# Kernel optimization log

Measured on AMD Instinct MI355X. Metric: run time of the kernel, lower is better.

Reference implementation:

```python
import jax, jax.numpy as jnp
import numpy as np

DIM = 192
HEADS = 6
WSIZE = (2, 8, 8)
SSIZE = (1, 4, 4)
HID = 768
EPS = 1e-5


def _rel_pos_index(ws):
    d, h, w = ws
    coords = np.stack(np.meshgrid(np.arange(d), np.arange(h), np.arange(w), indexing='ij'))
    cf = coords.reshape(3, -1)                       # (3, N)
    rel = (cf[:, :, None] - cf[:, None, :]).transpose(1, 2, 0)  # (N, N, 3)
    rel[:, :, 0] += d - 1
    rel[:, :, 1] += h - 1
    rel[:, :, 2] += w - 1
    rel[:, :, 0] *= (2 * h - 1) * (2 * w - 1)
    rel[:, :, 1] *= 2 * w - 1
    return rel.sum(-1)                               # (N, N) int


def _slices(w, s):
    if s == 0:
        return [slice(0, None)]
    return [slice(0, -w), slice(-w, -s), slice(-s, None)]


def _window_partition(x, ws):
    B, D, H, W, C = x.shape
    x = x.reshape(B, D // ws[0], ws[0], H // ws[1], ws[1], W // ws[2], ws[2], C)
    return x.transpose(0, 1, 3, 5, 2, 4, 6, 7).reshape(-1, ws[0] * ws[1] * ws[2], C)


def _window_reverse(win, ws, B, D, H, W):
    x = win.reshape(B, D // ws[0], H // ws[1], W // ws[2], ws[0], ws[1], ws[2], -1)
    return x.transpose(0, 1, 4, 2, 5, 3, 6, 7).reshape(B, D, H, W, -1)


def _compute_mask(D, H, W, ws, ss):
    img = np.zeros((1, D, H, W, 1), np.float32)
    cnt = 0
    for d in _slices(ws[0], ss[0]):
        for h in _slices(ws[1], ss[1]):
            for w in _slices(ws[2], ss[2]):
                img[:, d, h, w, :] = cnt
                cnt += 1
    x = img.reshape(1, D // ws[0], ws[0], H // ws[1], ws[1], W // ws[2], ws[2], 1)
    mw = x.transpose(0, 1, 3, 5, 2, 4, 6, 7).reshape(-1, ws[0] * ws[1] * ws[2])  # (nW, N)
    diff = mw[:, None, :] - mw[:, :, None]
    return np.where(diff != 0, np.float32(-100.0), np.float32(0.0))  # (nW, N, N)


def _ln(x, g, b):
    mu = x.mean(-1, keepdims=True)
    v = ((x - mu) ** 2).mean(-1, keepdims=True)
    return (x - mu) * jax.lax.rsqrt(v + EPS) * g + b


def setup_inputs() -> dict:
    key = jax.random.key(0)
    ks = jax.random.split(key, 8)
    C, H_, n_bias = DIM, HID, (2 * WSIZE[0] - 1) * (2 * WSIZE[1] - 1) * (2 * WSIZE[2] - 1)
    s = 0.02
    return {
        'x': jax.random.normal(ks[0], (2, 8, 64, 64, C), jnp.float32),
        'g1': jnp.ones((C,), jnp.float32), 'b1': jnp.zeros((C,), jnp.float32),
        'Wq': jax.random.normal(ks[1], (C, C), jnp.float32) * s,
        'Wkv': jax.random.normal(ks[2], (2 * C, C), jnp.float32) * s,
        'rpb': jax.random.normal(ks[3], (n_bias, HEADS), jnp.float32) * s,
        'Wp': jax.random.normal(ks[4], (C, C), jnp.float32) * s,
        'bp': jnp.zeros((C,), jnp.float32),
        'g2': jnp.ones((C,), jnp.float32), 'b2': jnp.zeros((C,), jnp.float32),
        'Wf1': jax.random.normal(ks[5], (H_, C), jnp.float32) * s,
        'bf1': jnp.zeros((H_,), jnp.float32),
        'Wf2': jax.random.normal(ks[6], (C, H_), jnp.float32) * s,
        'bf2': jnp.zeros((C,), jnp.float32),
    }


def reference(x, g1, b1, Wq, Wkv, rpb, Wp, bp, g2, b2, Wf1, bf1, Wf2, bf2):
    B, D, H, W, C = x.shape
    ws, ss = list(WSIZE), list(SSIZE)
    for i, sz in enumerate((D, H, W)):
        if sz <= ws[i]:
            ws[i], ss[i] = sz, 0
    shortcut = x
    x = _ln(x, g1, b1)
    # pad to window multiples
    pd, ph, pw = (-D) % ws[0], (-H) % ws[1], (-W) % ws[2]
    x = jnp.pad(x, ((0, 0), (0, pd), (0, ph), (0, pw), (0, 0)))
    Dp, Hp, Wp_ = D + pd, H + ph, W + pw
    shifted = any(s > 0 for s in ss)
    if shifted:
        x = jnp.roll(x, (-ss[0], -ss[1], -ss[2]), axis=(1, 2, 3))
        mask = jnp.asarray(_compute_mask(Dp, Hp, Wp_, ws, ss))  # (nW, N, N)
    xw = _window_partition(x, ws)                               # (B_, N, C)
    B_, N, _ = xw.shape
    hd = C // HEADS
    q = (xw @ Wq.T).reshape(B_, N, HEADS, hd).transpose(0, 2, 1, 3)      # (B_, h, N, hd)
    kv = (xw @ Wkv.T).reshape(B_, N, 2, HEADS, hd).transpose(2, 0, 3, 1, 4)
    k, v = kv[0], kv[1]
    attn = jnp.einsum('bhnd,bhmd->bhnm', q * (hd ** -0.5), k)            # (B_, h, N, N)
    idx = _rel_pos_index(tuple(ws))
    bias = rpb[idx.reshape(-1)].reshape(N, N, HEADS).transpose(2, 0, 1)  # (h, N, N)
    attn = attn + bias[None]
    if shifted:
        nW = mask.shape[0]
        attn = (attn.reshape(B_ // nW, nW, HEADS, N, N) + mask[None, :, None]).reshape(B_, HEADS, N, N)
    attn = jax.nn.softmax(attn, axis=-1)
    out = jnp.einsum('bhnm,bhmd->bhnd', attn, v).transpose(0, 2, 1, 3).reshape(B_, N, C)
    out = out @ Wp.T + bp
    x = _window_reverse(out, ws, B, Dp, Hp, Wp_)
    if shifted:
        x = jnp.roll(x, (ss[0], ss[1], ss[2]), axis=(1, 2, 3))
    x = x[:, :D, :H, :W]
    x = shortcut + x
    y = _ln(x, g2, b2)
    y = jax.nn.gelu(y @ Wf1.T + bf1, approximate=False) @ Wf2.T + bf2
    return x + y
```

## Files before the change

kernel.cpp:

```cpp
#include <hip/hip_runtime.h>
#include <cstdint>

#define DEVI static __device__ __forceinline__

typedef __attribute__((ext_vector_type(8))) short bf16x8;
typedef __attribute__((ext_vector_type(4))) float f32x4;
typedef __attribute__((ext_vector_type(8))) unsigned short ush8;

DEVI unsigned short f2bf(float f) {
    unsigned u = __float_as_uint(f);
    u += 0x7fff + ((u >> 16) & 1);
    return (unsigned short)(u >> 16);
}
DEVI float bf2f(unsigned short h) { return __uint_as_float(((unsigned)h) << 16); }

DEVI void gload16(const void* g, void* l) {
    __builtin_amdgcn_global_load_lds((const __attribute__((address_space(1))) void*)g,
                                     (__attribute__((address_space(3))) void*)l, 16, 0, 0);
}

DEVI float fast_gelu(float x) {
    float z = 1.5957691216057308f * (x + 0.044715f * x * x * x);
    return x - x * __builtin_amdgcn_rcpf(__expf(z) + 1.f);
}

__global__ __launch_bounds__(256) void k_pack(const float* __restrict__ Wq, const float* __restrict__ Wkv,
                                              const float* __restrict__ Wp, const float* __restrict__ Wf1,
                                              const float* __restrict__ Wf2, unsigned short* __restrict__ dst) {
    int t = blockIdx.x * 256 + threadIdx.x;
    if (t >= 55296) return;
    int c, base, K;
    const float* src = nullptr;
    if (t < 13824)      { c = t;         base = 0;      K = 192; }
    else if (t < 18432) { c = t - 13824; base = 110592; K = 192; src = Wp; }
    else if (t < 36864) { c = t - 18432; base = 147456; K = 192; src = Wf1; }
    else                { c = t - 36864; base = 294912; K = 768; src = Wf2; }
    int lane = c & 63, fk = c >> 6, Kf = K >> 5;
    int kf = fk % Kf, nf = fk / Kf;
    int row = nf * 16 + (lane & 15), col = kf * 32 + (lane >> 4) * 8;
    ush8 o;
    if (t < 13824) {
        if (row < 192) {
            #pragma unroll
            for (int q = 0; q < 8; q++) o[q] = f2bf(Wq[row * 192 + col + q] * 0.17677669529663687f);
        } else {
            #pragma unroll
            for (int q = 0; q < 8; q++) o[q] = f2bf(Wkv[(row - 192) * 192 + col + q]);
        }
    } else {
        #pragma unroll
        for (int q = 0; q < 8; q++) o[q] = f2bf(src[(long)row * K + col + q]);
    }
    *(ush8*)&dst[base + c * 8] = o;
}

__global__ __launch_bounds__(256) void k_bmt(const float* __restrict__ rpb, float* __restrict__ bmt) {
    int t = blockIdx.x * 256 + threadIdx.x;
    int h = t >> 17;
    int r = t & 131071;
    int v = r >> 14;
    int ij = r & 16383;
    int i = ij >> 7, li = (ij >> 3) & 15, fn = ij & 7;
    int j = fn * 16 + li;
    int tdi = i >> 6, thi = (i >> 3) & 7, twi = i & 7;
    int tdj = j >> 6, thj = (j >> 3) & 7, twj = j & 7;
    int idx = ((tdi - tdj + 1) * 15 + (thi - thj + 7)) * 15 + (twi - twj + 7);
    float b = rpb[idx * 6 + h];
    int dwb = v & 1, hwb = (v >> 1) & 1, wwb = (v >> 2) & 1;
    int ri = (dwb ? 1 + tdi : 0) * 9 + (hwb ? (thi < 4 ? 1 : 2) : 0) * 3 + (wwb ? (twi < 4 ? 1 : 2) : 0);
    int rj = (dwb ? 1 + tdj : 0) * 9 + (hwb ? (thj < 4 ? 1 : 2) : 0) * 3 + (wwb ? (twj < 4 ? 1 : 2) : 0);
    if (ri != rj) b -= 100.f;
    bmt[(long)(h * 8 + v) * 16384 + i * 128 + li * 8 + fn] = b;
}

__global__ __launch_bounds__(256) void k_ln(const float* __restrict__ x, const float* __restrict__ g,
                                            const float* __restrict__ b, unsigned short* __restrict__ outp) {
    int wid = threadIdx.x >> 6, lane = threadIdx.x & 63;
    int t = blockIdx.x * 4 + wid;
    int w = t >> 7, tt = t & 127;
    int bb = w >> 8, rem = w & 255;
    int dw = rem >> 6, hw = (rem >> 3) & 7, ww = rem & 7;
    int td = tt >> 6, th = (tt >> 3) & 7, tw = tt & 7;
    int d = (dw * 2 + td + 1) & 7;
    int hh = (hw * 8 + th + 4) & 63;
    int wo = (ww * 8 + tw + 4) & 63;
    long src = (long)((bb * 8 + d) * 64 + hh) * 64 + wo;
    const float* xp = x + src * 192;
    float v0 = xp[lane], v1 = xp[lane + 64], v2 = xp[lane + 128];
    float s = v0 + v1 + v2, ss = v0 * v0 + v1 * v1 + v2 * v2;
    #pragma unroll
    for (int m = 32; m; m >>= 1) { s += __shfl_xor(s, m); ss += __shfl_xor(ss, m); }
    float mu = s * (1.f / 192.f);
    float var = ss * (1.f / 192.f) - mu * mu;
    float inv = rsqrtf(var + 1e-5f);
    unsigned short* op = outp + (long)t * 192;
    op[lane]       = f2bf((v0 - mu) * inv * g[lane]       + b[lane]);
    op[lane + 64]  = f2bf((v1 - mu) * inv * g[lane + 64]  + b[lane + 64]);
    op[lane + 128] = f2bf((v2 - mu) * inv * g[lane + 128] + b[lane + 128]);
}

template <int EPI>
__global__ __launch_bounds__(256, 4) void k_gemm(const unsigned short* __restrict__ A,
                                                 const unsigned short* __restrict__ Bpk, int K,
                                                 const float* __restrict__ bias,
                                                 const float* __restrict__ addsrc,
                                                 unsigned short* __restrict__ outU) {
    __shared__ __align__(16) unsigned short As[2][256 * 32];
    int tid = threadIdx.x;
    int wid = tid >> 6, lane = tid & 63;
    int g = lane >> 4, li = lane & 15;
    int m0 = blockIdx.y * 256, n0 = blockIdx.x * 64;
    int Kf = K >> 5;

    f32x4 acc[4][4];
    #pragma unroll
    for (int i = 0; i < 4; i++)
        #pragma unroll
        for (int j = 0; j < 4; j++) acc[i][j] = (f32x4){0.f, 0.f, 0.f, 0.f};

    int sg = ((tid & 3) ^ ((tid >> 3) & 3)) * 8;
    const unsigned short* pa = A + (long)(m0 + (tid >> 2)) * K + sg;
    const unsigned short* pbk = Bpk + ((long)(n0 >> 4) * Kf * 64 + lane) * 8;

#define STAGE(buf, kt) do { \
    _Pragma("unroll") \
    for (int c = 0; c < 4; c++) \
        gload16(pa + (long)(c * 64) * K + (kt), &As[buf][c * 2048 + tid * 8]); \
} while (0)

    STAGE(0, 0);
    __syncthreads();

    int cur = 0;
    int acol = (g ^ ((li >> 1) & 3)) * 8;
    for (int t = 0; t < Kf; t++) {
        bf16x8 bfr[4];
        #pragma unroll
        for (int j = 0; j < 4; j++)
            bfr[j] = *(const bf16x8*)(pbk + ((long)j * Kf + t) * 512);
        if (t + 1 < Kf) STAGE(cur ^ 1, (t + 1) << 5);
        const unsigned short* ab = &As[cur][(wid * 64 + li) * 32 + acol];
        bf16x8 af[4];
        #pragma unroll
        for (int i = 0; i < 4; i++) af[i] = *(const bf16x8*)(ab + i * 512);
        __builtin_amdgcn_s_setprio(1);
        #pragma unroll
        for (int i = 0; i < 4; i++)
            #pragma unroll
            for (int j = 0; j < 4; j++)
                acc[i][j] = __builtin_amdgcn_mfma_f32_16x16x32_bf16(af[i], bfr[j], acc[i][j], 0, 0, 0);
        __builtin_amdgcn_s_setprio(0);
        if (t + 1 < Kf) {
            __syncthreads();
            cur ^= 1;
        }
    }
#undef STAGE

    #pragma unroll
    for (int i = 0; i < 4; i++) {
        int rowb = m0 + wid * 64 + i * 16 + g * 4;
        #pragma unroll
        for (int j = 0; j < 4; j++) {
            int col = n0 + j * 16 + li;
            #pragma unroll
            for (int r = 0; r < 4; r++) {
                float v = acc[i][j][r];
                int rr = rowb + r;
                {
                    int w = rr >> 7, tt = rr & 127;
                    int bb2 = w >> 8, rem = w & 255;
                    int dw = rem >> 6, hw = (rem >> 3) & 7, ww = rem & 7;
                    int td = tt >> 6, th = (tt >> 3) & 7, tw = tt & 7;
                    int d = (dw * 2 + td + 1) & 7;
                    int hh = (hw * 8 + th + 4) & 63;
                    int wo = (ww * 8 + tw + 4) & 63;
                    long src = ((long)((bb2 * 8 + d) * 64 + hh) * 64 + wo) * 192 + col;
                    outU[src] = f2bf(addsrc[src] + v + bias[col]);
                }
            }
        }
    }
}

__global__ __launch_bounds__(512, 4) void k_mlp(const unsigned short* __restrict__ x1,
                                                const float* __restrict__ g2, const float* __restrict__ b2,
                                                const unsigned short* __restrict__ wf1pk,
                                                const unsigned short* __restrict__ wf2pk,
                                                const float* __restrict__ bf1v, const float* __restrict__ bf2v,
                                                float* __restrict__ out) {
    __shared__ __align__(16) unsigned short A_s[24 * 512];
    __shared__ __align__(16) unsigned short H_s[16 * 512];
    int tid = threadIdx.x;
    int wid = tid >> 6, lane = tid & 63;
    int g = lane >> 4, li = lane & 15;
    long r0 = (long)blockIdx.x * 64;

    {
        int row = tid >> 3;
        int c0 = (tid & 7) * 24;
        const unsigned short* xp = x1 + (r0 + row) * 192 + c0;
        float v[24];
        #pragma unroll
        for (int q = 0; q < 3; q++) {
            ush8 f = *(const ush8*)(xp + q * 8);
            #pragma unroll
            for (int e = 0; e < 8; e++) v[q * 8 + e] = bf2f(f[e]);
        }
        float s = 0.f, ss = 0.f;
        #pragma unroll
        for (int q = 0; q < 24; q++) { s += v[q]; ss += v[q] * v[q]; }
        #pragma unroll
        for (int m = 1; m < 8; m <<= 1) { s += __shfl_xor(s, m); ss += __shfl_xor(ss, m); }
        float mu = s * (1.f / 192.f);
        float var = ss * (1.f / 192.f) - mu * mu;
        float inv = rsqrtf(var + 1e-5f);
        ush8 o[3];
        #pragma unroll
        for (int q = 0; q < 24; q++) {
            float gv = g2[c0 + q], bv = b2[c0 + q];
            o[q >> 3][q & 7] = f2bf((v[q] - mu) * inv * gv + bv);
        }
        #pragma unroll
        for (int q = 0; q < 3; q++) {
            int cb = c0 + q * 8;
            int fi = (row >> 4) * 6 + (cb >> 5);
            int l2 = (((cb >> 3) & 3) << 4) | (row & 15);
            *(ush8*)&A_s[(fi * 64 + l2) * 8] = o[q];
        }
    }
    __syncthreads();

    int mw = wid >> 2, nw = wid & 3;
    int kf2 = wid >> 1;
    int gpos = ((wid & 1) << 1) | (li >> 3);
    int e = li & 7;
    f32x4 acc2[2][3];
    #pragma unroll
    for (int i = 0; i < 2; i++)
        #pragma unroll
        for (int j = 0; j < 3; j++) acc2[i][j] = (f32x4){0.f, 0.f, 0.f, 0.f};

    for (int ch = 0; ch < 6; ch++) {
        f32x4 acc1[4];
        #pragma unroll
        for (int i = 0; i < 4; i++) acc1[i] = (f32x4){0.f, 0.f, 0.f, 0.f};
        int nf = ch * 8 + wid;
        float bv1 = bf1v[ch * 128 + wid * 16 + li];
        #pragma unroll
        for (int kf = 0; kf < 6; kf++) {
            bf16x8 b = *(const bf16x8*)&wf1pk[(((long)nf * 6 + kf) * 64 + lane) * 8];
            __builtin_amdgcn_s_setprio(1);
            #pragma unroll
            for (int mf = 0; mf < 4; mf++) {
                bf16x8 a = *(const bf16x8*)&A_s[(((mf * 6 + kf) * 64) + lane) * 8];
                acc1[mf] = __builtin_amdgcn_mfma_f32_16x16x32_bf16(a, b, acc1[mf], 0, 0, 0);
            }
            __builtin_amdgcn_s_setprio(0);
        }
        bf16x8 w2p[2][3];
        #pragma unroll
        for (int kf = 0; kf < 2; kf++)
            #pragma unroll
            for (int jf = 0; jf < 3; jf++)
                w2p[kf][jf] = *(const bf16x8*)&wf2pk[(((long)(nw * 3 + jf) * 24 + ch * 4 + kf) * 64 + lane) * 8];
        #pragma unroll
        for (int mf = 0; mf < 4; mf++)
            #pragma unroll
            for (int r = 0; r < 4; r++) {
                int l2 = (gpos << 4) | (g * 4 + r);
                H_s[((mf * 4 + kf2) * 64 + l2) * 8 + e] = f2bf(fast_gelu(acc1[mf][r] + bv1));
            }
        __syncthreads();
        #pragma unroll
        for (int kf = 0; kf < 4; kf++) {
            bf16x8 hf[2], bf[3];
            #pragma unroll
            for (int mf = 0; mf < 2; mf++)
                hf[mf] = *(const bf16x8*)&H_s[(((mw * 2 + mf) * 4 + kf) * 64 + lane) * 8];
            if (kf < 2) {
                #pragma unroll
                for (int jf = 0; jf < 3; jf++) bf[jf] = w2p[kf][jf];
            } else {
                #pragma unroll
                for (int jf = 0; jf < 3; jf++)
                    bf[jf] = *(const bf16x8*)&wf2pk[(((long)(nw * 3 + jf) * 24 + ch * 4 + kf) * 64 + lane) * 8];
            }
            __builtin_amdgcn_s_setprio(1);
            #pragma unroll
            for (int mf = 0; mf < 2; mf++)
                #pragma unroll
                for (int jf = 0; jf < 3; jf++)
                    acc2[mf][jf] = __builtin_amdgcn_mfma_f32_16x16x32_bf16(hf[mf], bf[jf], acc2[mf][jf], 0, 0, 0);
            __builtin_amdgcn_s_setprio(0);
        }
        __syncthreads();
    }

    #pragma unroll
    for (int mf = 0; mf < 2; mf++) {
        #pragma unroll
        for (int jf = 0; jf < 3; jf++) {
            int col = nw * 48 + jf * 16 + li;
            float bv = bf2v[col];
            #pragma unroll
            for (int r = 0; r < 4; r++) {
                int row = mw * 32 + mf * 16 + g * 4 + r;
                long idx = (r0 + row) * 192 + col;
                out[idx] = bf2f(x1[idx]) + acc2[mf][jf][r] + bv;
            }
        }
    }
}

__global__ __launch_bounds__(256, 2) void k_attn(const unsigned short* __restrict__ xw,
                                                 const unsigned short* __restrict__ qkvpk,
                                                 const float* __restrict__ bmt,
                                                 unsigned short* __restrict__ attnout) {
    __shared__ __align__(16) char smem[78336];
    unsigned short* xw_s = (unsigned short*)smem;
    unsigned short* p_s  = (unsigned short*)smem;
    unsigned short* q_s  = (unsigned short*)(smem + 51200);
    unsigned short* k_s  = (unsigned short*)(smem + 60416);
    unsigned short* vt_s = (unsigned short*)(smem + 69632);

    int b = blockIdx.x;
    int xcd = b & 7, j = b >> 3;
    int w = xcd + 8 * (j / 6), h = j % 6;
    int tid = threadIdx.x, wid = tid >> 6, lane = tid & 63, g = lane >> 4, li = lane & 15;
    int rem = w & 255;
    int dw = rem >> 6, hw = (rem >> 3) & 7, ww = rem & 7;
    int variant = (dw == 3 ? 1 : 0) | (hw == 7 ? 2 : 0) | (ww == 7 ? 4 : 0);
    const float* bm = bmt + (long)(h * 8 + variant) * 16384;

    {
        int r = tid >> 1, c0 = (tid & 1) * 96;
        const unsigned short* src = xw + ((long)w * 128 + r) * 192 + c0;
        #pragma unroll
        for (int jj = 0; jj < 12; jj++)
            *(uint4*)&xw_s[r * 200 + c0 + jj * 8] = *(const uint4*)(src + jj * 8);
    }
    __syncthreads();

    f32x4 qk[2][6];
    #pragma unroll
    for (int i = 0; i < 2; i++)
        #pragma unroll
        for (int jj = 0; jj < 6; jj++) qk[i][jj] = (f32x4){0.f, 0.f, 0.f, 0.f};
    bf16x8 bwc[6];
    #pragma unroll
    for (int jj = 0; jj < 6; jj++) {
        int nf = (jj >> 1) * 12 + 2 * h + (jj & 1);
        bwc[jj] = *(const bf16x8*)&qkvpk[(((long)nf * 6 + 0) * 64 + lane) * 8];
    }
    #pragma unroll
    for (int kf = 0; kf < 6; kf++) {
        bf16x8 a0 = *(const bf16x8*)&xw_s[(wid * 32 + li) * 200 + kf * 32 + g * 8];
        bf16x8 a1 = *(const bf16x8*)&xw_s[(wid * 32 + 16 + li) * 200 + kf * 32 + g * 8];
        bf16x8 bwn[6];
        if (kf < 5) {
            #pragma unroll
            for (int jj = 0; jj < 6; jj++) {
                int nf = (jj >> 1) * 12 + 2 * h + (jj & 1);
                bwn[jj] = *(const bf16x8*)&qkvpk[(((long)nf * 6 + (kf + 1)) * 64 + lane) * 8];
            }
        }
        __builtin_amdgcn_s_setprio(1);
        #pragma unroll
        for (int jj = 0; jj < 6; jj++) {
            qk[0][jj] = __builtin_amdgcn_mfma_f32_16x16x32_bf16(a0, bwc[jj], qk[0][jj], 0, 0, 0);
            qk[1][jj] = __builtin_amdgcn_mfma_f32_16x16x32_bf16(a1, bwc[jj], qk[1][jj], 0, 0, 0);
        }
        __builtin_amdgcn_s_setprio(0);
        if (kf < 5) {
            #pragma unroll
            for (int jj = 0; jj < 6; jj++) bwc[jj] = bwn[jj];
        }
    }
    #pragma unroll
    for (int mf = 0; mf < 2; mf++) {
        int tokb = wid * 32 + mf * 16 + g * 4;
        #pragma unroll
        for (int r = 0; r < 4; r++) {
            int tok = tokb + r;
            q_s[tok * 36 + li]          = f2bf(qk[mf][0][r]);
            q_s[tok * 36 + 16 + li]     = f2bf(qk[mf][1][r]);
            k_s[tok * 36 + li]          = f2bf(qk[mf][2][r]);
            k_s[tok * 36 + 16 + li]     = f2bf(qk[mf][3][r]);
            vt_s[li * 136 + tok]        = f2bf(qk[mf][4][r]);
            vt_s[(16 + li) * 136 + tok] = f2bf(qk[mf][5][r]);
        }
    }
    __syncthreads();

    f32x4 s[2][8];
    #pragma unroll
    for (int i = 0; i < 2; i++)
        #pragma unroll
        for (int jj = 0; jj < 8; jj++) s[i][jj] = (f32x4){0.f, 0.f, 0.f, 0.f};
    bf16x8 qa[2];
    #pragma unroll
    for (int fm = 0; fm < 2; fm++)
        qa[fm] = *(const bf16x8*)&q_s[(wid * 32 + fm * 16 + li) * 36 + g * 8];
    __builtin_amdgcn_s_setprio(1);
    #pragma unroll
    for (int fn = 0; fn < 8; fn++) {
        bf16x8 kb = *(const bf16x8*)&k_s[(fn * 16 + li) * 36 + g * 8];
        s[0][fn] = __builtin_amdgcn_mfma_f32_16x16x32_bf16(qa[0], kb, s[0][fn], 0, 0, 0);
        s[1][fn] = __builtin_amdgcn_mfma_f32_16x16x32_bf16(qa[1], kb, s[1][fn], 0, 0, 0);
    }
    __builtin_amdgcn_s_setprio(0);

    #pragma unroll
    for (int fm = 0; fm < 2; fm++) {
        #pragma unroll
        for (int r = 0; r < 4; r++) {
            int i = wid * 32 + fm * 16 + g * 4 + r;
            const float4 b0 = *(const float4*)&bm[i * 128 + li * 8];
            const float4 b1 = *(const float4*)&bm[i * 128 + li * 8 + 4];
            float vals[8];
            vals[0] = s[fm][0][r] + b0.x; vals[1] = s[fm][1][r] + b0.y;
            vals[2] = s[fm][2][r] + b0.z; vals[3] = s[fm][3][r] + b0.w;
            vals[4] = s[fm][4][r] + b1.x; vals[5] = s[fm][5][r] + b1.y;
            vals[6] = s[fm][6][r] + b1.z; vals[7] = s[fm][7][r] + b1.w;
            float mx = fmaxf(fmaxf(fmaxf(vals[0], vals[1]), fmaxf(vals[2], vals[3])),
                             fmaxf(fmaxf(vals[4], vals[5]), fmaxf(vals[6], vals[7])));
            #pragma unroll
            for (int m = 1; m < 16; m <<= 1) mx = fmaxf(mx, __shfl_xor(mx, m, 16));
            float sum = 0.f;
            #pragma unroll
            for (int fn = 0; fn < 8; fn++) { vals[fn] = __expf(vals[fn] - mx); sum += vals[fn]; }
            #pragma unroll
            for (int m = 1; m < 16; m <<= 1) sum += __shfl_xor(sum, m, 16);
            float inv = __builtin_amdgcn_rcpf(sum);
            #pragma unroll
            for (int fn = 0; fn < 8; fn++)
                p_s[i * 132 + fn * 16 + li] = f2bf(vals[fn] * inv);
        }
    }

    f32x4 o[2][2];
    #pragma unroll
    for (int i = 0; i < 2; i++)
        #pragma unroll
        for (int jj = 0; jj < 2; jj++) o[i][jj] = (f32x4){0.f, 0.f, 0.f, 0.f};
    __builtin_amdgcn_s_setprio(1);
    #pragma unroll
    for (int ks = 0; ks < 4; ks++) {
        bf16x8 pa[2];
        #pragma unroll
        for (int fm = 0; fm < 2; fm++)
            pa[fm] = *(const bf16x8*)&p_s[(wid * 32 + fm * 16 + li) * 132 + ks * 32 + g * 8];
        #pragma unroll
        for (int fn = 0; fn < 2; fn++) {
            bf16x8 vb = *(const bf16x8*)&vt_s[(fn * 16 + li) * 136 + ks * 32 + g * 8];
            o[0][fn] = __builtin_amdgcn_mfma_f32_16x16x32_bf16(pa[0], vb, o[0][fn], 0, 0, 0);
            o[1][fn] = __builtin_amdgcn_mfma_f32_16x16x32_bf16(pa[1], vb, o[1][fn], 0, 0, 0);
        }
    }
    __builtin_amdgcn_s_setprio(0);

    unsigned short* op = attnout + (long)w * 128 * 192 + h * 32;
    #pragma unroll
    for (int fm = 0; fm < 2; fm++) {
        #pragma unroll
        for (int fn = 0; fn < 2; fn++) {
            #pragma unroll
            for (int r = 0; r < 4; r++) {
                int n = wid * 32 + fm * 16 + g * 4 + r;
                op[(long)n * 192 + fn * 16 + li] = f2bf(o[fm][fn][r]);
            }
        }
    }
}

extern "C" void kernel_launch(void* const* d_in, const int* in_sizes, int n_in,
                              void* d_out, int out_size, void* d_ws, size_t ws_size,
                              hipStream_t stream) {
    const float* x   = (const float*)d_in[0];
    const float* g1  = (const float*)d_in[1];
    const float* b1  = (const float*)d_in[2];
    const float* Wq  = (const float*)d_in[3];
    const float* Wkv = (const float*)d_in[4];
    const float* rpb = (const float*)d_in[5];
    const float* Wp  = (const float*)d_in[6];
    const float* bp  = (const float*)d_in[7];
    const float* g2  = (const float*)d_in[8];
    const float* b2  = (const float*)d_in[9];
    const float* Wf1 = (const float*)d_in[10];
    const float* bf1 = (const float*)d_in[11];
    const float* Wf2 = (const float*)d_in[12];
    const float* bf2 = (const float*)d_in[13];
    float* out = (float*)d_out;
    char* ws = (char*)d_ws;

    unsigned short* wpk  = (unsigned short*)ws;
    float* bmt           = (float*)(ws + 917504);
    unsigned short* xw   = (unsigned short*)(ws + 4194304);
    unsigned short* attb = (unsigned short*)(ws + 29360128);
    unsigned short* x1b  = (unsigned short*)(ws + 54525952);

    const unsigned short* qkvpk = wpk;
    const unsigned short* wppk  = wpk + 110592;
    const unsigned short* wf1pk = wpk + 147456;
    const unsigned short* wf2pk = wpk + 294912;

    k_pack<<<216, 256, 0, stream>>>(Wq, Wkv, Wp, Wf1, Wf2, wpk);
    k_bmt<<<3072, 256, 0, stream>>>(rpb, bmt);
    k_ln<<<16384, 256, 0, stream>>>(x, g1, b1, xw);
    k_attn<<<3072, 256, 0, stream>>>(xw, qkvpk, bmt, attb);
    k_gemm<1><<<dim3(3, 256), 256, 0, stream>>>(attb, wppk, 192, bp, x, x1b);
    k_mlp<<<1024, 512, 0, stream>>>(x1b, g2, b2, wf1pk, wf2pk, bf1, bf2, out);
}
```

Baseline: 182.7 us.

## Write LN output in MFMA fragment layout and load attention A operands directly

The layernorm kernel now writes its bf16 output pre-packed into MFMA A-fragment order. The attention kernel can then read the QKV-projection operands straight from global memory into registers, with prefetch, instead of staging the whole 128x192 window in shared memory. Q, K, V^T and P now use packed fragment layouts in LDS, so each fragment read is one contiguous 16-byte load per lane. Shared memory per block drops from about 78KB to about 48KB and the launch bound goes from 2 to 3 blocks per CU to allow more occupancy. In exchange, the LN stores become scattered 2-byte writes, and the A operands are read repeatedly from global memory or cache.

```diff
diff --git a/kernel.cpp b/kernel.cpp
--- a/kernel.cpp
+++ b/kernel.cpp
@@ -74,7 +74,7 @@
 }
 
 __global__ __launch_bounds__(256) void k_ln(const float* __restrict__ x, const float* __restrict__ g,
-                                            const float* __restrict__ b, unsigned short* __restrict__ outp) {
+                                            const float* __restrict__ b, unsigned short* __restrict__ xwpk) {
     int wid = threadIdx.x >> 6, lane = threadIdx.x & 63;
     int t = blockIdx.x * 4 + wid;
     int w = t >> 7, tt = t & 127;
@@ -93,10 +93,15 @@
     float mu = s * (1.f / 192.f);
     float var = ss * (1.f / 192.f) - mu * mu;
     float inv = rsqrtf(var + 1e-5f);
-    unsigned short* op = outp + (long)t * 192;
-    op[lane]       = f2bf((v0 - mu) * inv * g[lane]       + b[lane]);
-    op[lane + 64]  = f2bf((v1 - mu) * inv * g[lane + 64]  + b[lane + 64]);
-    op[lane + 128] = f2bf((v2 - mu) * inv * g[lane + 128] + b[lane + 128]);
+    int mfq = tt >> 4, rowf = tt & 15;
+    long base = ((long)w * 48 + mfq * 6) * 512;
+    #pragma unroll
+    for (int q = 0; q < 3; q++) {
+        int c = lane + q * 64;
+        float vv = (q == 0 ? v0 : (q == 1 ? v1 : v2));
+        float y = (vv - mu) * inv * g[c] + b[c];
+        xwpk[base + (c >> 5) * 512 + ((((c >> 3) & 3) << 4) + rowf) * 8 + (c & 7)] = f2bf(y);
+    }
 }
 
 template <int EPI>
@@ -313,40 +318,31 @@
     }
 }
 
-__global__ __launch_bounds__(256, 2) void k_attn(const unsigned short* __restrict__ xw,
+__global__ __launch_bounds__(256, 3) void k_attn(const unsigned short* __restrict__ xwpk,
                                                  const unsigned short* __restrict__ qkvpk,
                                                  const float* __restrict__ bmt,
                                                  unsigned short* __restrict__ attnout) {
-    __shared__ __align__(16) char smem[78336];
-    unsigned short* xw_s = (unsigned short*)smem;
-    unsigned short* p_s  = (unsigned short*)smem;
-    unsigned short* q_s  = (unsigned short*)(smem + 51200);
-    unsigned short* k_s  = (unsigned short*)(smem + 60416);
-    unsigned short* vt_s = (unsigned short*)(smem + 69632);
+    __shared__ __align__(16) unsigned short p_pk[32 * 512];
+    __shared__ __align__(16) unsigned short k_pk[8 * 512];
+    __shared__ __align__(16) unsigned short vt_pk[8 * 512];
 
     int b = blockIdx.x;
-    int xcd = b & 7, j = b >> 3;
-    int w = xcd + 8 * (j / 6), h = j % 6;
+    int xcd = b & 7, jd = b >> 3;
+    int w = xcd + 8 * (jd / 6), h = jd % 6;
     int tid = threadIdx.x, wid = tid >> 6, lane = tid & 63, g = lane >> 4, li = lane & 15;
     int rem = w & 255;
     int dw = rem >> 6, hw = (rem >> 3) & 7, ww = rem & 7;
     int variant = (dw == 3 ? 1 : 0) | (hw == 7 ? 2 : 0) | (ww == 7 ? 4 : 0);
     const float* bm = bmt + (long)(h * 8 + variant) * 16384;
-
-    {
-        int r = tid >> 1, c0 = (tid & 1) * 96;
-        const unsigned short* src = xw + ((long)w * 128 + r) * 192 + c0;
-        #pragma unroll
-        for (int jj = 0; jj < 12; jj++)
-            *(uint4*)&xw_s[r * 200 + c0 + jj * 8] = *(const uint4*)(src + jj * 8);
-    }
-    __syncthreads();
+    const unsigned short* xwb = xwpk + (long)w * 48 * 512;
 
     f32x4 qk[2][6];
     #pragma unroll
     for (int i = 0; i < 2; i++)
         #pragma unroll
         for (int jj = 0; jj < 6; jj++) qk[i][jj] = (f32x4){0.f, 0.f, 0.f, 0.f};
+    bf16x8 a0c = *(const bf16x8*)&xwb[(((wid * 2 + 0) * 6 + 0) * 64 + lane) * 8];
+    bf16x8 a1c = *(const bf16x8*)&xwb[(((wid * 2 + 1) * 6 + 0) * 64 + lane) * 8];
     bf16x8 bwc[6];
     #pragma unroll
     for (int jj = 0; jj < 6; jj++) {
@@ -355,10 +351,10 @@
     }
     #pragma unroll
     for (int kf = 0; kf < 6; kf++) {
-        bf16x8 a0 = *(const bf16x8*)&xw_s[(wid * 32 + li) * 200 + kf * 32 + g * 8];
-        bf16x8 a1 = *(const bf16x8*)&xw_s[(wid * 32 + 16 + li) * 200 + kf * 32 + g * 8];
-        bf16x8 bwn[6];
+        bf16x8 a0n, a1n, bwn[6];
         if (kf < 5) {
+            a0n = *(const bf16x8*)&xwb[(((wid * 2 + 0) * 6 + kf + 1) * 64 + lane) * 8];
+            a1n = *(const bf16x8*)&xwb[(((wid * 2 + 1) * 6 + kf + 1) * 64 + lane) * 8];
             #pragma unroll
             for (int jj = 0; jj < 6; jj++) {
                 int nf = (jj >> 1) * 12 + 2 * h + (jj & 1);
@@ -368,44 +364,44 @@
         __builtin_amdgcn_s_setprio(1);
         #pragma unroll
         for (int jj = 0; jj < 6; jj++) {
-            qk[0][jj] = __builtin_amdgcn_mfma_f32_16x16x32_bf16(a0, bwc[jj], qk[0][jj], 0, 0, 0);
-            qk[1][jj] = __builtin_amdgcn_mfma_f32_16x16x32_bf16(a1, bwc[jj], qk[1][jj], 0, 0, 0);
+            qk[0][jj] = __builtin_amdgcn_mfma_f32_16x16x32_bf16(a0c, bwc[jj], qk[0][jj], 0, 0, 0);
+            qk[1][jj] = __builtin_amdgcn_mfma_f32_16x16x32_bf16(a1c, bwc[jj], qk[1][jj], 0, 0, 0);
         }
         __builtin_amdgcn_s_setprio(0);
         if (kf < 5) {
+            a0c = a0n; a1c = a1n;
             #pragma unroll
             for (int jj = 0; jj < 6; jj++) bwc[jj] = bwn[jj];
         }
     }
-    #pragma unroll
-    for (int mf = 0; mf < 2; mf++) {
-        int tokb = wid * 32 + mf * 16 + g * 4;
+
+    #pragma unroll
+    for (int fm = 0; fm < 2; fm++) {
         #pragma unroll
         for (int r = 0; r < 4; r++) {
-            int tok = tokb + r;
-            q_s[tok * 36 + li]          = f2bf(qk[mf][0][r]);
-            q_s[tok * 36 + 16 + li]     = f2bf(qk[mf][1][r]);
-            k_s[tok * 36 + li]          = f2bf(qk[mf][2][r]);
-            k_s[tok * 36 + 16 + li]     = f2bf(qk[mf][3][r]);
-            vt_s[li * 136 + tok]        = f2bf(qk[mf][4][r]);
-            vt_s[(16 + li) * 136 + tok] = f2bf(qk[mf][5][r]);
+            int ll = g * 4 + r;
+            p_pk[((wid * 8 + fm) * 64 + ((0 + (li >> 3)) << 4) + ll) * 8 + (li & 7)] = f2bf(qk[fm][0][r]);
+            p_pk[((wid * 8 + fm) * 64 + ((2 + (li >> 3)) << 4) + ll) * 8 + (li & 7)] = f2bf(qk[fm][1][r]);
+            k_pk[((wid * 2 + fm) * 64 + ((0 + (li >> 3)) << 4) + ll) * 8 + (li & 7)] = f2bf(qk[fm][2][r]);
+            k_pk[((wid * 2 + fm) * 64 + ((2 + (li >> 3)) << 4) + ll) * 8 + (li & 7)] = f2bf(qk[fm][3][r]);
+            vt_pk[((0 * 4 + wid) * 64 + ((fm * 2 + (g >> 1)) << 4) + li) * 8 + ((g & 1) * 4 + r)] = f2bf(qk[fm][4][r]);
+            vt_pk[((1 * 4 + wid) * 64 + ((fm * 2 + (g >> 1)) << 4) + li) * 8 + ((g & 1) * 4 + r)] = f2bf(qk[fm][5][r]);
         }
     }
     __syncthreads();
 
+    bf16x8 qa[2];
+    qa[0] = *(const bf16x8*)&p_pk[((wid * 8 + 0) * 64 + lane) * 8];
+    qa[1] = *(const bf16x8*)&p_pk[((wid * 8 + 1) * 64 + lane) * 8];
     f32x4 s[2][8];
     #pragma unroll
     for (int i = 0; i < 2; i++)
         #pragma unroll
         for (int jj = 0; jj < 8; jj++) s[i][jj] = (f32x4){0.f, 0.f, 0.f, 0.f};
-    bf16x8 qa[2];
-    #pragma unroll
-    for (int fm = 0; fm < 2; fm++)
-        qa[fm] = *(const bf16x8*)&q_s[(wid * 32 + fm * 16 + li) * 36 + g * 8];
     __builtin_amdgcn_s_setprio(1);
     #pragma unroll
     for (int fn = 0; fn < 8; fn++) {
-        bf16x8 kb = *(const bf16x8*)&k_s[(fn * 16 + li) * 36 + g * 8];
+        bf16x8 kb = *(const bf16x8*)&k_pk[(fn * 64 + lane) * 8];
         s[0][fn] = __builtin_amdgcn_mfma_f32_16x16x32_bf16(qa[0], kb, s[0][fn], 0, 0, 0);
         s[1][fn] = __builtin_amdgcn_mfma_f32_16x16x32_bf16(qa[1], kb, s[1][fn], 0, 0, 0);
     }
@@ -433,9 +429,11 @@
             #pragma unroll
             for (int m = 1; m < 16; m <<= 1) sum += __shfl_xor(sum, m, 16);
             float inv = __builtin_amdgcn_rcpf(sum);
+            int ll = g * 4 + r;
             #pragma unroll
             for (int fn = 0; fn < 8; fn++)
-                p_s[i * 132 + fn * 16 + li] = f2bf(vals[fn] * inv);
+                p_pk[((wid * 8 + fm * 4 + (fn >> 1)) * 64 + ((((fn & 1) << 1) + (li >> 3)) << 4) + ll) * 8 + (li & 7)]
+                    = f2bf(vals[fn] * inv);
         }
     }
 
@@ -450,10 +448,10 @@
         bf16x8 pa[2];
         #pragma unroll
         for (int fm = 0; fm < 2; fm++)
-            pa[fm] = *(const bf16x8*)&p_s[(wid * 32 + fm * 16 + li) * 132 + ks * 32 + g * 8];
+            pa[fm] = *(const bf16x8*)&p_pk[((wid * 8 + fm * 4 + ks) * 64 + lane) * 8];
         #pragma unroll
         for (int fn = 0; fn < 2; fn++) {
-            bf16x8 vb = *(const bf16x8*)&vt_s[(fn * 16 + li) * 136 + ks * 32 + g * 8];
+            bf16x8 vb = *(const bf16x8*)&vt_pk[((fn * 4 + ks) * 64 + lane) * 8];
             o[0][fn] = __builtin_amdgcn_mfma_f32_16x16x32_bf16(pa[0], vb, o[0][fn], 0, 0, 0);
             o[1][fn] = __builtin_amdgcn_mfma_f32_16x16x32_bf16(pa[1], vb, o[1][fn], 0, 0, 0);
         }
@@ -496,7 +494,7 @@
 
     unsigned short* wpk  = (unsigned short*)ws;
     float* bmt           = (float*)(ws + 917504);
-    unsigned short* xw   = (unsigned short*)(ws + 4194304);
+    unsigned short* xwp  = (unsigned short*)(ws + 4194304);
     unsigned short* attb = (unsigned short*)(ws + 29360128);
     unsigned short* x1b  = (unsigned short*)(ws + 54525952);
 
@@ -507,8 +505,8 @@
 
     k_pack<<<216, 256, 0, stream>>>(Wq, Wkv, Wp, Wf1, Wf2, wpk);
     k_bmt<<<3072, 256, 0, stream>>>(rpb, bmt);
-    k_ln<<<16384, 256, 0, stream>>>(x, g1, b1, xw);
-    k_attn<<<3072, 256, 0, stream>>>(xw, qkvpk, bmt, attb);
+    k_ln<<<16384, 256, 0, stream>>>(x, g1, b1, xwp);
+    k_attn<<<3072, 256, 0, stream>>>(xwp, qkvpk, bmt, attb);
     k_gemm<1><<<dim3(3, 256), 256, 0, stream>>>(attb, wppk, 192, bp, x, x1b);
     k_mlp<<<1024, 512, 0, stream>>>(x1b, g2, b2, wf1pk, wf2pk, bf1, bf2, out);
 }
```

Result: faster. 156.8 us (median of 3 runs) (-14.2%).
